# Kernel optimization log

Measured on AMD Instinct MI355X. Metric: run time of the kernel, lower is better.

The kernel has to match this reference:

```python
import jax, jax.numpy as jnp
import numpy as np

H = 512
S = 65  # 64 board cells + appended constant 1


def _heads(y, wk, wq, wv):
    # y: [H, S]; wk/wq/wv: [3, H, H] -> atts: [3, S, H]
    def one(wk_i, wq_i, wv_i):
        k = wk_i @ y            # [H, S]
        q = wq_i @ y            # [H, S]
        v = wv_i @ y            # [H, S]
        sm = jax.nn.softmax(k.T @ q, axis=1)  # [S, S], softmax over dim=1
        return sm @ v.T         # [S, H]
    return jax.vmap(one)(wk, wq, wv)


def setup_inputs() -> dict:
    key = jax.random.key(0)
    ks = jax.random.split(key, 10)
    r = lambda k, s: jax.random.normal(k, s, dtype=jnp.float32)
    return {
        "inputs": r(ks[0], (1, 64)),
        "embedding": r(ks[1], (H, S)),
        "wq": r(ks[2], (3, 3, H, H)),
        "wk": r(ks[3], (3, 3, H, H)),
        "wv": r(ks[4], (3, 3, H, H)),
        "linear1": r(ks[5], (3 * H, H)),
        "linear2": r(ks[6], (3 * H, H)),
        "linear3": r(ks[7], (3 * H, 2 * H)),
        "linear4": r(ks[8], (2 * H, H)),
        "linear5": r(ks[9], (H, 64)),
    }


def reference(inputs, embedding, wq, wk, wv, linear1, linear2, linear3, linear4, linear5):
    x = jnp.concatenate([inputs[0], jnp.ones((1,), inputs.dtype)])  # [S]
    y = embedding * x  # [H, S] (broadcast over rows)

    # Layer 1 (3 heads)
    a1 = _heads(y, wk[0], wq[0], wv[0])  # [3, S, H]
    y = jax.nn.relu(jnp.concatenate([a1[0], a1[1], a1[2]], axis=1) @ linear1).T  # [H, S]

    # Layer 2 -- NOTE: original code cats att11, att12, att23 (a bug we preserve)
    a2 = _heads(y, wk[1], wq[1], wv[1])
    y = jax.nn.relu(jnp.concatenate([a1[0], a1[1], a2[2]], axis=1) @ linear2).T  # [H, S]

    # Layer 3 -- NOTE: original code cats att11, att12, att33 (preserved)
    a3 = _heads(y, wk[2], wq[2], wv[2])
    y = jax.nn.relu(jnp.concatenate([a1[0], a1[1], a3[2]], axis=1) @ linear3)[64]  # [2H]

    # dropout p=0.1 -> identity in eval mode
    y = jnp.tanh(y @ linear4)  # [H]
    score = y @ linear5        # [64]
    return score[None, :]      # [1, 64]
```

## Files before the change

kernel.cpp:

```cpp
#include <hip/hip_runtime.h>
#include <hip/hip_bf16.h>
#include <math.h>

#define H 512
#define S 65
#define SP 80
#define HS (H * S)
#define PHS (H * SP)
#define KS3 24
#define KS4 16


__global__ void scale_embed_kernel(const float* __restrict__ inp,
                                   const float* __restrict__ emb,
                                   float* __restrict__ yT) {
    int i = blockIdx.x * blockDim.x + threadIdx.x;
    if (i < PHS) {
        int s = i / H;
        int h = i % H;
        float v = 0.f;
        if (s < S) {
            float x = (s == 64) ? 1.0f : inp[s];
            v = emb[h * S + s] * x;
        }
        yT[i] = v;
    }
}

__device__ __forceinline__ void mac4(float4& c, float ax, float ay, float az,
                                     float aw, const float4& w0, const float4& w1,
                                     const float4& w2, const float4& w3) {
    c.x = fmaf(ax, w0.x, c.x); c.y = fmaf(ax, w0.y, c.y);
    c.z = fmaf(ax, w0.z, c.z); c.w = fmaf(ax, w0.w, c.w);
    c.x = fmaf(ay, w1.x, c.x); c.y = fmaf(ay, w1.y, c.y);
    c.z = fmaf(ay, w1.z, c.z); c.w = fmaf(ay, w1.w, c.w);
    c.x = fmaf(az, w2.x, c.x); c.y = fmaf(az, w2.y, c.y);
    c.z = fmaf(az, w2.z, c.z); c.w = fmaf(az, w2.w, c.w);
    c.x = fmaf(aw, w3.x, c.x); c.y = fmaf(aw, w3.y, c.y);
    c.z = fmaf(aw, w3.z, c.z); c.w = fmaf(aw, w3.w, c.w);
}

__global__ void __launch_bounds__(256, 1)
kqv_gemm_tiled(const float* __restrict__ wq,
               const float* __restrict__ wk,
               const float* __restrict__ wv,
               int mat0,
               const float* __restrict__ yT,
               float* __restrict__ part) {
    int slot  = blockIdx.z;
    int which = blockIdx.y;
    int mat = mat0 + slot;
    const float* W = (which == 0 ? wk : (which == 1 ? wq : wv)) + (size_t)mat * H * H;

    int n0   = (blockIdx.x & 15) * 32;
    int kidx = blockIdx.x >> 4;

    __shared__ float Wt[64 * 32];
    __shared__ float As[SP * 68];

    int t  = threadIdx.x;
    int nq = t & 7;
    int g  = t >> 3;
    bool r2 = (g < 16);

    float4 acc0 = {0,0,0,0}, acc1 = {0,0,0,0}, acc2 = {0,0,0,0};

    for (int ch = 0; ch < 4; ++ch) {
        int kc0 = kidx * 256 + ch * 64;
#pragma unroll
        for (int c = 0; c < 2; ++c) {
            int f = c * 256 + t;
            int wn  = f >> 4;
            int kf4 = f & 15;
            float4 w4 = *(const float4*)(W + (size_t)(n0 + wn) * H + kc0 + 4 * kf4);
            int sw = ((wn >> 2) ^ (kf4 & 7));
            int base = (4 * kf4) * 32 + 4 * sw + (wn & 3);
            Wt[base     ] = w4.x;
            Wt[base + 32] = w4.y;
            Wt[base + 64] = w4.z;
            Wt[base + 96] = w4.w;
        }
#pragma unroll
        for (int c = 0; c < 5; ++c) {
            int f = c * 256 + t;
            int as  = f >> 4;
            int kf4 = f & 15;
            *(float4*)(&As[as * 68 + 4 * kf4]) =
                *(const float4*)(yT + (size_t)as * H + kc0 + 4 * kf4);
        }
        __syncthreads();

#pragma unroll
        for (int k4 = 0; k4 < 16; ++k4) {
            int swc = 4 * (nq ^ (k4 & 7));
            float4 w0 = *(const float4*)(&Wt[(4 * k4 + 0) * 32 + swc]);
            float4 w1 = *(const float4*)(&Wt[(4 * k4 + 1) * 32 + swc]);
            float4 w2 = *(const float4*)(&Wt[(4 * k4 + 2) * 32 + swc]);
            float4 w3 = *(const float4*)(&Wt[(4 * k4 + 3) * 32 + swc]);
            {
                float4 a = *(const float4*)(&As[g * 68 + 4 * k4]);
                mac4(acc0, a.x, a.y, a.z, a.w, w0, w1, w2, w3);
            }
            {
                float4 a = *(const float4*)(&As[(g + 32) * 68 + 4 * k4]);
                mac4(acc1, a.x, a.y, a.z, a.w, w0, w1, w2, w3);
            }
            if (r2) {
                float4 a = *(const float4*)(&As[(g + 64) * 68 + 4 * k4]);
                mac4(acc2, a.x, a.y, a.z, a.w, w0, w1, w2, w3);
            }
        }
        __syncthreads();
    }

    float* P = part + (size_t)((slot * 3 + which) * 2 + kidx) * PHS;
    *(float4*)(P + (size_t)g * H + n0 + 4 * nq) = acc0;
    *(float4*)(P + (size_t)(g + 32) * H + n0 + 4 * nq) = acc1;
    if (r2) *(float4*)(P + (size_t)(g + 64) * H + n0 + 4 * nq) = acc2;
}

__device__ __forceinline__ float score_part(const float* __restrict__ Q0,
                                            const float* __restrict__ Q1,
                                            const float* __restrict__ ka,
                                            int b, int t) {
    const float4* q0 = (const float4*)(Q0 + (size_t)b * H) + t * 32;
    const float4* q1 = (const float4*)(Q1 + (size_t)b * H) + t * 32;
    const float4* kl = (const float4*)ka + t * 32;
    float4 c0 = {0,0,0,0}, c1 = {0,0,0,0};
#pragma unroll
    for (int u = 0; u < 32; u += 2) {
        float4 qa = q0[u], qb = q1[u], k0 = kl[u];
        float4 qc = q0[u+1], qd = q1[u+1], k1 = kl[u+1];
        c0.x = fmaf(k0.x, qa.x + qb.x, c0.x);
        c0.y = fmaf(k0.y, qa.y + qb.y, c0.y);
        c0.z = fmaf(k0.z, qa.z + qb.z, c0.z);
        c0.w = fmaf(k0.w, qa.w + qb.w, c0.w);
        c1.x = fmaf(k1.x, qc.x + qd.x, c1.x);
        c1.y = fmaf(k1.y, qc.y + qd.y, c1.y);
        c1.z = fmaf(k1.z, qc.z + qd.z, c1.z);
        c1.w = fmaf(k1.w, qc.w + qd.w, c1.w);
    }
    return ((c0.x + c0.y) + (c0.z + c0.w)) + ((c1.x + c1.y) + (c1.z + c1.w));
}

__global__ void attn_kernel(const float* __restrict__ kqvp,
                            float* __restrict__ att) {
    int a = blockIdx.x;
    int slot = blockIdx.y;
    int tid = threadIdx.x;

    const float* base = kqvp + (size_t)slot * 6 * PHS;
    const float* K0 = base;
    const float* K1 = base + PHS;
    const float* Q0 = base + 2 * (size_t)PHS;
    const float* Q1 = base + 3 * (size_t)PHS;
    const float* V0 = base + 4 * (size_t)PHS;
    const float* V1 = base + 5 * (size_t)PHS;
    float* ao = att + (size_t)slot * PHS + (size_t)a * H;

    __shared__ float ka[H];
    __shared__ float sp[4 * 65];
    __shared__ float smv[S];
    __shared__ float p[S];

    ka[tid]       = K0[(size_t)a * H + tid]       + K1[(size_t)a * H + tid];
    ka[tid + 256] = K0[(size_t)a * H + tid + 256] + K1[(size_t)a * H + tid + 256];
    __syncthreads();

    {
        int b = tid & 63;
        int t = tid >> 6;
        sp[t * 65 + b] = score_part(Q0, Q1, ka, b, t);
        if (tid < 4) sp[tid * 65 + 64] = score_part(Q0, Q1, ka, 64, tid);
    }
    __syncthreads();

    if (tid < S) {
        smv[tid] = (sp[tid] + sp[65 + tid]) + (sp[130 + tid] + sp[195 + tid]);
    }
    __syncthreads();

    float maxv = -INFINITY;
    for (int i = 0; i < S; ++i) maxv = fmaxf(maxv, smv[i]);
    float sum = 0.0f;
    for (int i = 0; i < S; ++i) sum += expf(smv[i] - maxv);
    float inv = 1.0f / sum;
    if (tid < S) p[tid] = expf(smv[tid] - maxv) * inv;
    __syncthreads();

#pragma unroll
    for (int rep = 0; rep < 2; ++rep) {
        int hh = tid + rep * 256;
        float a0 = 0.f, a1 = 0.f;
#pragma unroll 4
        for (int b = 0; b < 64; b += 2) {
            a0 = fmaf(p[b    ], V0[(size_t)(b    ) * H + hh] + V1[(size_t)(b    ) * H + hh], a0);
            a1 = fmaf(p[b + 1], V0[(size_t)(b + 1) * H + hh] + V1[(size_t)(b + 1) * H + hh], a1);
        }
        a0 = fmaf(p[64], V0[(size_t)64 * H + hh] + V1[(size_t)64 * H + hh], a0);
        ao[hh] = a0 + a1;
    }
}

__device__ __forceinline__ void lin4row_dev(const float* __restrict__ att,
                                            int col0,
                                            const float* __restrict__ L,
                                            float* __restrict__ dst,
                                            int s0, int tid) {
    __shared__ float Ar[4 * 256];
    __shared__ float4 red[4 * 128];

    {
        int rr = tid >> 6;
        int cc = tid & 63;
        *(float4*)(&Ar[rr * 256 + cc * 4]) =
            *(const float4*)(att + (size_t)(s0 + rr) * H + col0 + cc * 4);
    }
    __syncthreads();

    int h4 = (tid & 127) * 4;
    int jh = tid >> 7;
    const float* Lj = L + (size_t)(jh * 128) * H + h4;
    const float* A0 = Ar + jh * 128;

    float4 c0 = {0,0,0,0}, c1 = {0,0,0,0}, c2 = {0,0,0,0}, c3 = {0,0,0,0};
#pragma unroll 8
    for (int j = 0; j < 128; ++j) {
        float4 L4 = *(const float4*)(Lj + (size_t)j * H);
        float a0 = A0[j], a1 = A0[256 + j], a2 = A0[512 + j], a3 = A0[768 + j];
        c0.x = fmaf(a0, L4.x, c0.x); c0.y = fmaf(a0, L4.y, c0.y);
        c0.z = fmaf(a0, L4.z, c0.z); c0.w = fmaf(a0, L4.w, c0.w);
        c1.x = fmaf(a1, L4.x, c1.x); c1.y = fmaf(a1, L4.y, c1.y);
        c1.z = fmaf(a1, L4.z, c1.z); c1.w = fmaf(a1, L4.w, c1.w);
        c2.x = fmaf(a2, L4.x, c2.x); c2.y = fmaf(a2, L4.y, c2.y);
        c2.z = fmaf(a2, L4.z, c2.z); c2.w = fmaf(a2, L4.w, c2.w);
        c3.x = fmaf(a3, L4.x, c3.x); c3.y = fmaf(a3, L4.y, c3.y);
        c3.z = fmaf(a3, L4.z, c3.z); c3.w = fmaf(a3, L4.w, c3.w);
    }

    if (jh == 1) {
        int x = tid & 127;
        red[x] = c0; red[128 + x] = c1; red[256 + x] = c2; red[384 + x] = c3;
    }
    __syncthreads();
    if (jh == 0) {
        float4 r0 = red[tid], r1 = red[128 + tid], r2 = red[256 + tid], r3 = red[384 + tid];
        c0.x += r0.x; c0.y += r0.y; c0.z += r0.z; c0.w += r0.w;
        c1.x += r1.x; c1.y += r1.y; c1.z += r1.z; c1.w += r1.w;
        c2.x += r2.x; c2.y += r2.y; c2.z += r2.z; c2.w += r2.w;
        c3.x += r3.x; c3.y += r3.y; c3.z += r3.z; c3.w += r3.w;
        *(float4*)(dst + (size_t)(s0 + 0) * H + h4) = c0;
        *(float4*)(dst + (size_t)(s0 + 1) * H + h4) = c1;
        *(float4*)(dst + (size_t)(s0 + 2) * H + h4) = c2;
        *(float4*)(dst + (size_t)(s0 + 3) * H + h4) = c3;
    }
}

__global__ void mega_lin_kernel(const float* __restrict__ att1,
                                const float* __restrict__ lin1,
                                const float* __restrict__ lin2,
                                const float* __restrict__ lin3,
                                float* __restrict__ plin1,
                                float* __restrict__ plin2,
                                float* __restrict__ tpart) {
    int bx = blockIdx.x;
    int tid = threadIdx.x;

    if (bx < 170) {
        int seg = bx / 17;
        int p   = bx % 17;
        const float* att;
        const float* L;
        float* dst;
        if (seg < 6) {
            att = att1 + (size_t)(seg >> 1) * PHS;
            L   = lin1 + (size_t)(seg * 256) * H;
            dst = plin1 + (size_t)seg * PHS;
        } else {
            int s2 = seg - 6;
            att = att1 + (size_t)(s2 >> 1) * PHS;
            L   = lin2 + (size_t)(s2 * 256) * H;
            dst = plin2 + (size_t)s2 * PHS;
        }
        lin4row_dev(att, (seg & 1) * 256, L, dst, p * 4, tid);
    } else {
        int idx = bx - 170;
        int j2 = (idx & 3) * 256 + tid;
        int ks = idx >> 2;
        const float* row = att1 + (size_t)(ks >> 3) * PHS + (size_t)64 * H;
        int j0 = (ks & 7) * 64;
        int jbase = ks * 64;
        float a0 = 0.f, a1 = 0.f, a2 = 0.f, a3 = 0.f;
        for (int j = 0; j < 64; j += 4) {
            a0 = fmaf(row[j0 + j + 0], lin3[(size_t)(jbase + j + 0) * 1024 + j2], a0);
            a1 = fmaf(row[j0 + j + 1], lin3[(size_t)(jbase + j + 1) * 1024 + j2], a1);
            a2 = fmaf(row[j0 + j + 2], lin3[(size_t)(jbase + j + 2) * 1024 + j2], a2);
            a3 = fmaf(row[j0 + j + 3], lin3[(size_t)(jbase + j + 3) * 1024 + j2], a3);
        }
        tpart[ks * 1024 + j2] = (a0 + a1) + (a2 + a3);
    }
}

__global__ void lin2c_kernel(const float* __restrict__ att2,
                             const float* __restrict__ lin2,
                             float* __restrict__ plin2) {
    int seg = 4 + blockIdx.x / 17;
    int p   = blockIdx.x % 17;
    lin4row_dev(att2, (seg & 1) * 256, lin2 + (size_t)(seg * 256) * H,
                plin2 + (size_t)seg * PHS, p * 4, threadIdx.x);
}

__global__ void combine6_relu_kernel(const float* __restrict__ part,
                                     float* __restrict__ yT) {
    int i = blockIdx.x * 256 + threadIdx.x;
    float s = 0.f;
#pragma unroll
    for (int p = 0; p < 6; ++p) s += part[(size_t)p * PHS + i];
    yT[i] = fmaxf(s, 0.0f);
}

__global__ void attn3_lin3c_kernel(const float* __restrict__ kqvp,
                                   const float* __restrict__ lin3,
                                   float* __restrict__ tpart) {
    int tid = threadIdx.x;
    int ks  = 16 + blockIdx.y;
    int j2  = blockIdx.x * 256 + tid;
    int j0  = (ks & 7) * 64;

    const float* K0 = kqvp;
    const float* K1 = kqvp + PHS;
    const float* Q0 = kqvp + 2 * (size_t)PHS;
    const float* Q1 = kqvp + 3 * (size_t)PHS;
    const float* V0 = kqvp + 4 * (size_t)PHS;
    const float* V1 = kqvp + 5 * (size_t)PHS;

    __shared__ float ka[H];
    __shared__ float sp[4 * 65];
    __shared__ float smv[S];
    __shared__ float p[S];
    __shared__ float att_s[64];

    ka[tid]       = K0[(size_t)64 * H + tid]       + K1[(size_t)64 * H + tid];
    ka[tid + 256] = K0[(size_t)64 * H + tid + 256] + K1[(size_t)64 * H + tid + 256];
    __syncthreads();

    {
        int b = tid & 63;
        int t = tid >> 6;
        sp[t * 65 + b] = score_part(Q0, Q1, ka, b, t);
        if (tid < 4) sp[tid * 65 + 64] = score_part(Q0, Q1, ka, 64, tid);
    }
    __syncthreads();

    if (tid < S) {
        smv[tid] = (sp[tid] + sp[65 + tid]) + (sp[130 + tid] + sp[195 + tid]);
    }
    __syncthreads();

    float maxv = -INFINITY;
    for (int i = 0; i < S; ++i) maxv = fmaxf(maxv, smv[i]);
    float sum = 0.0f;
    for (int i = 0; i < S; ++i) sum += expf(smv[i] - maxv);
    float inv = 1.0f / sum;
    if (tid < S) p[tid] = expf(smv[tid] - maxv) * inv;
    __syncthreads();

    if (tid < 64) {
        int hh = j0 + tid;
        float a0 = 0.f, a1 = 0.f;
#pragma unroll 4
        for (int b = 0; b < 64; b += 2) {
            a0 = fmaf(p[b    ], V0[(size_t)(b    ) * H + hh] + V1[(size_t)(b    ) * H + hh], a0);
            a1 = fmaf(p[b + 1], V0[(size_t)(b + 1) * H + hh] + V1[(size_t)(b + 1) * H + hh], a1);
        }
        a0 = fmaf(p[64], V0[(size_t)64 * H + hh] + V1[(size_t)64 * H + hh], a0);
        att_s[tid] = a0 + a1;
    }
    __syncthreads();

    int jbase = ks * 64;
    float a0 = 0.f, a1 = 0.f, a2 = 0.f, a3 = 0.f;
    for (int j = 0; j < 64; j += 4) {
        a0 = fmaf(att_s[j + 0], lin3[(size_t)(jbase + j + 0) * 1024 + j2], a0);
        a1 = fmaf(att_s[j + 1], lin3[(size_t)(jbase + j + 1) * 1024 + j2], a1);
        a2 = fmaf(att_s[j + 2], lin3[(size_t)(jbase + j + 2) * 1024 + j2], a2);
        a3 = fmaf(att_s[j + 3], lin3[(size_t)(jbase + j + 3) * 1024 + j2], a3);
    }
    tpart[ks * 1024 + j2] = (a0 + a1) + (a2 + a3);
}

__global__ void lin4_partial_kernel(const float* __restrict__ tpart,
                                    const float* __restrict__ lin4,
                                    float* __restrict__ upart) {
    __shared__ float tl[64];
    int hh = blockIdx.x * 256 + threadIdx.x;
    int ks = blockIdx.y;
    int j2base = ks * 64;

    if (threadIdx.x < 64) {
        int j2 = j2base + threadIdx.x;
        float s = 0.f;
#pragma unroll
        for (int p = 0; p < KS3; ++p) s += tpart[p * 1024 + j2];
        tl[threadIdx.x] = fmaxf(s, 0.f);
    }
    __syncthreads();

    float a0 = 0.f, a1 = 0.f, a2 = 0.f, a3 = 0.f;
    for (int j = 0; j < 64; j += 4) {
        a0 = fmaf(tl[j + 0], lin4[(size_t)(j2base + j + 0) * H + hh], a0);
        a1 = fmaf(tl[j + 1], lin4[(size_t)(j2base + j + 1) * H + hh], a1);
        a2 = fmaf(tl[j + 2], lin4[(size_t)(j2base + j + 2) * H + hh], a2);
        a3 = fmaf(tl[j + 3], lin4[(size_t)(j2base + j + 3) * H + hh], a3);
    }
    upart[ks * H + hh] = (a0 + a1) + (a2 + a3);
}

__global__ void final_out_kernel(const float* __restrict__ upart,
                                 const float* __restrict__ lin5,
                                 float* __restrict__ out) {
    __shared__ float u[H];
    __shared__ float pr[8][64];
    int tid = threadIdx.x;

    {
        float s = 0.f;
#pragma unroll
        for (int p = 0; p < KS4; ++p) s += upart[p * H + tid];
        u[tid] = tanhf(s);
    }
    __syncthreads();

    int o  = tid & 63;
    int sl = tid >> 6;
    float acc = 0.f;
    int h0 = sl * 64;
#pragma unroll 8
    for (int j = 0; j < 64; ++j) {
        acc = fmaf(u[h0 + j], lin5[(h0 + j) * 64 + o], acc);
    }
    pr[sl][o] = acc;
    __syncthreads();

    if (tid < 64) {
        float s = 0.f;
#pragma unroll
        for (int p = 0; p < 8; ++p) s += pr[p][tid];
        out[tid] = s;
    }
}

extern "C" void kernel_launch(void* const* d_in, const int* in_sizes, int n_in,
                              void* d_out, int out_size, void* d_ws, size_t ws_size,
                              hipStream_t stream) {
    const float* inputs  = (const float*)d_in[0];
    const float* emb     = (const float*)d_in[1];
    const float* wq      = (const float*)d_in[2];
    const float* wk      = (const float*)d_in[3];
    const float* wv      = (const float*)d_in[4];
    const float* linear1 = (const float*)d_in[5];
    const float* linear2 = (const float*)d_in[6];
    const float* linear3 = (const float*)d_in[7];
    const float* linear4 = (const float*)d_in[8];
    const float* linear5 = (const float*)d_in[9];
    float* out = (float*)d_out;

    float* ws    = (float*)d_ws;
    float* y     = ws;
    float* kqvp  = y     + PHS;
    float* att1  = kqvp  + 18 * PHS;
    float* att2  = att1  + 3 * PHS;
    float* plin1 = att2  + PHS;
    float* plin2 = plin1 + 6 * PHS;
    float* tpart = plin2 + 6 * PHS;
    float* upart = tpart + KS3 * 1024;

    const int nb  = HS / 256;
    const int nbp = PHS / 256;

    scale_embed_kernel<<<nbp, 256, 0, stream>>>(inputs, emb, y);

    kqv_gemm_tiled<<<dim3(32, 3, 3), 256, 0, stream>>>(wq, wk, wv, 0, y, kqvp);
    attn_kernel<<<dim3(S, 3), 256, 0, stream>>>(kqvp, att1);
    mega_lin_kernel<<<234, 256, 0, stream>>>(att1, linear1, linear2, linear3,
                                             plin1, plin2, tpart);
    combine6_relu_kernel<<<nb, 256, 0, stream>>>(plin1, y);

    kqv_gemm_tiled<<<dim3(32, 3, 1), 256, 0, stream>>>(wq, wk, wv, 5, y, kqvp);
    attn_kernel<<<dim3(S, 1), 256, 0, stream>>>(kqvp, att2);
    lin2c_kernel<<<34, 256, 0, stream>>>(att2, linear2, plin2);
    combine6_relu_kernel<<<nb, 256, 0, stream>>>(plin2, y);

    kqv_gemm_tiled<<<dim3(32, 3, 1), 256, 0, stream>>>(wq, wk, wv, 8, y, kqvp);
    attn3_lin3c_kernel<<<dim3(4, 8), 256, 0, stream>>>(kqvp, linear3, tpart);

    lin4_partial_kernel<<<dim3(2, KS4), 256, 0, stream>>>(tpart, linear4, upart);
    final_out_kernel<<<1, 512, 0, stream>>>(upart, linear5, out);
}
```

Measured before the change: 254.8 us.

## Drop K-split for layer-1 KQV GEMM and fuse lin2 tail with combine

```diff
diff --git a/kernel.cpp b/kernel.cpp
--- a/kernel.cpp
+++ b/kernel.cpp
@@ -40,6 +40,7 @@
     c.z = fmaf(aw, w3.z, c.z); c.w = fmaf(aw, w3.w, c.w);
 }
 
+template <int KSPLIT>
 __global__ void __launch_bounds__(256, 1)
 kqv_gemm_tiled(const float* __restrict__ wq,
                const float* __restrict__ wk,
@@ -54,6 +55,7 @@
 
     int n0   = (blockIdx.x & 15) * 32;
     int kidx = blockIdx.x >> 4;
+    const int NCH = 8 / KSPLIT;
 
     __shared__ float Wt[64 * 32];
     __shared__ float As[SP * 68];
@@ -65,8 +67,8 @@
 
     float4 acc0 = {0,0,0,0}, acc1 = {0,0,0,0}, acc2 = {0,0,0,0};
 
-    for (int ch = 0; ch < 4; ++ch) {
-        int kc0 = kidx * 256 + ch * 64;
+    for (int ch = 0; ch < NCH; ++ch) {
+        int kc0 = (kidx * NCH + ch) * 64;
 #pragma unroll
         for (int c = 0; c < 2; ++c) {
             int f = c * 256 + t;
@@ -113,49 +115,54 @@
         __syncthreads();
     }
 
-    float* P = part + (size_t)((slot * 3 + which) * 2 + kidx) * PHS;
+    float* P = part + (size_t)((slot * 3 + which) * KSPLIT + kidx) * PHS;
     *(float4*)(P + (size_t)g * H + n0 + 4 * nq) = acc0;
     *(float4*)(P + (size_t)(g + 32) * H + n0 + 4 * nq) = acc1;
     if (r2) *(float4*)(P + (size_t)(g + 64) * H + n0 + 4 * nq) = acc2;
 }
 
-__device__ __forceinline__ float score_part(const float* __restrict__ Q0,
-                                            const float* __restrict__ Q1,
+template <int NS>
+__device__ __forceinline__ float score_part(const float* __restrict__ Q,
                                             const float* __restrict__ ka,
                                             int b, int t) {
-    const float4* q0 = (const float4*)(Q0 + (size_t)b * H) + t * 32;
-    const float4* q1 = (const float4*)(Q1 + (size_t)b * H) + t * 32;
+    const float4* q0 = (const float4*)(Q + (size_t)b * H) + t * 32;
+    const float4* q1 = (const float4*)(Q + PHS + (size_t)b * H) + t * 32;
     const float4* kl = (const float4*)ka + t * 32;
     float4 c0 = {0,0,0,0}, c1 = {0,0,0,0};
 #pragma unroll
     for (int u = 0; u < 32; u += 2) {
-        float4 qa = q0[u], qb = q1[u], k0 = kl[u];
-        float4 qc = q0[u+1], qd = q1[u+1], k1 = kl[u+1];
-        c0.x = fmaf(k0.x, qa.x + qb.x, c0.x);
-        c0.y = fmaf(k0.y, qa.y + qb.y, c0.y);
-        c0.z = fmaf(k0.z, qa.z + qb.z, c0.z);
-        c0.w = fmaf(k0.w, qa.w + qb.w, c0.w);
-        c1.x = fmaf(k1.x, qc.x + qd.x, c1.x);
-        c1.y = fmaf(k1.y, qc.y + qd.y, c1.y);
-        c1.z = fmaf(k1.z, qc.z + qd.z, c1.z);
-        c1.w = fmaf(k1.w, qc.w + qd.w, c1.w);
+        float4 qa = q0[u], qc = q0[u + 1];
+        float4 k0 = kl[u], k1 = kl[u + 1];
+        if (NS == 2) {
+            float4 qb = q1[u], qd = q1[u + 1];
+            qa.x += qb.x; qa.y += qb.y; qa.z += qb.z; qa.w += qb.w;
+            qc.x += qd.x; qc.y += qd.y; qc.z += qd.z; qc.w += qd.w;
+        }
+        c0.x = fmaf(k0.x, qa.x, c0.x);
+        c0.y = fmaf(k0.y, qa.y, c0.y);
+        c0.z = fmaf(k0.z, qa.z, c0.z);
+        c0.w = fmaf(k0.w, qa.w, c0.w);
+        c1.x = fmaf(k1.x, qc.x, c1.x);
+        c1.y = fmaf(k1.y, qc.y, c1.y);
+        c1.z = fmaf(k1.z, qc.z, c1.z);
+        c1.w = fmaf(k1.w, qc.w, c1.w);
     }
     return ((c0.x + c0.y) + (c0.z + c0.w)) + ((c1.x + c1.y) + (c1.z + c1.w));
 }
 
+template <int NS>
 __global__ void attn_kernel(const float* __restrict__ kqvp,
                             float* __restrict__ att) {
     int a = blockIdx.x;
     int slot = blockIdx.y;
     int tid = threadIdx.x;
 
-    const float* base = kqvp + (size_t)slot * 6 * PHS;
+    const float* base = kqvp + (size_t)slot * 3 * NS * PHS;
     const float* K0 = base;
-    const float* K1 = base + PHS;
-    const float* Q0 = base + 2 * (size_t)PHS;
-    const float* Q1 = base + 3 * (size_t)PHS;
-    const float* V0 = base + 4 * (size_t)PHS;
-    const float* V1 = base + 5 * (size_t)PHS;
+    const float* Q0 = base + (size_t)NS * PHS;
+    const float* V0 = base + (size_t)2 * NS * PHS;
+    const float* K1 = K0 + PHS;
+    const float* V1 = V0 + PHS;
     float* ao = att + (size_t)slot * PHS + (size_t)a * H;
 
     __shared__ float ka[H];
@@ -163,15 +170,20 @@
     __shared__ float smv[S];
     __shared__ float p[S];
 
-    ka[tid]       = K0[(size_t)a * H + tid]       + K1[(size_t)a * H + tid];
-    ka[tid + 256] = K0[(size_t)a * H + tid + 256] + K1[(size_t)a * H + tid + 256];
+    if (NS == 2) {
+        ka[tid]       = K0[(size_t)a * H + tid]       + K1[(size_t)a * H + tid];
+        ka[tid + 256] = K0[(size_t)a * H + tid + 256] + K1[(size_t)a * H + tid + 256];
+    } else {
+        ka[tid]       = K0[(size_t)a * H + tid];
+        ka[tid + 256] = K0[(size_t)a * H + tid + 256];
+    }
     __syncthreads();
 
     {
         int b = tid & 63;
         int t = tid >> 6;
-        sp[t * 65 + b] = score_part(Q0, Q1, ka, b, t);
-        if (tid < 4) sp[tid * 65 + 64] = score_part(Q0, Q1, ka, 64, tid);
+        sp[t * 65 + b] = score_part<NS>(Q0, ka, b, t);
+        if (tid < 4) sp[tid * 65 + 64] = score_part<NS>(Q0, ka, 64, tid);
     }
     __syncthreads();
 
@@ -194,10 +206,20 @@
         float a0 = 0.f, a1 = 0.f;
 #pragma unroll 4
         for (int b = 0; b < 64; b += 2) {
-            a0 = fmaf(p[b    ], V0[(size_t)(b    ) * H + hh] + V1[(size_t)(b    ) * H + hh], a0);
-            a1 = fmaf(p[b + 1], V0[(size_t)(b + 1) * H + hh] + V1[(size_t)(b + 1) * H + hh], a1);
-        }
-        a0 = fmaf(p[64], V0[(size_t)64 * H + hh] + V1[(size_t)64 * H + hh], a0);
+            float v0 = V0[(size_t)(b    ) * H + hh];
+            float v1 = V0[(size_t)(b + 1) * H + hh];
+            if (NS == 2) {
+                v0 += V1[(size_t)(b    ) * H + hh];
+                v1 += V1[(size_t)(b + 1) * H + hh];
+            }
+            a0 = fmaf(p[b    ], v0, a0);
+            a1 = fmaf(p[b + 1], v1, a1);
+        }
+        {
+            float v0 = V0[(size_t)64 * H + hh];
+            if (NS == 2) v0 += V1[(size_t)64 * H + hh];
+            a0 = fmaf(p[64], v0, a0);
+        }
         ao[hh] = a0 + a1;
     }
 }
@@ -301,15 +323,6 @@
     }
 }
 
-__global__ void lin2c_kernel(const float* __restrict__ att2,
-                             const float* __restrict__ lin2,
-                             float* __restrict__ plin2) {
-    int seg = 4 + blockIdx.x / 17;
-    int p   = blockIdx.x % 17;
-    lin4row_dev(att2, (seg & 1) * 256, lin2 + (size_t)(seg * 256) * H,
-                plin2 + (size_t)seg * PHS, p * 4, threadIdx.x);
-}
-
 __global__ void combine6_relu_kernel(const float* __restrict__ part,
                                      float* __restrict__ yT) {
     int i = blockIdx.x * 256 + threadIdx.x;
@@ -317,6 +330,35 @@
 #pragma unroll
     for (int p = 0; p < 6; ++p) s += part[(size_t)p * PHS + i];
     yT[i] = fmaxf(s, 0.0f);
+}
+
+__global__ void lin2c_combine_kernel(const float* __restrict__ att2,
+                                     const float* __restrict__ lin2,
+                                     const float* __restrict__ plin2,
+                                     float* __restrict__ yT) {
+    int i = blockIdx.x * 256 + threadIdx.x;
+    int s = i / H;
+    int h = i % H;
+    const float* row = att2 + (size_t)s * H;
+    const float* L4 = lin2 + (size_t)1024 * H + h;
+    const float* L5 = lin2 + (size_t)1280 * H + h;
+
+    float a0 = 0.f, a1 = 0.f, a2 = 0.f, a3 = 0.f;
+    for (int j = 0; j < 256; j += 4) {
+        a0 = fmaf(row[j + 0], L4[(size_t)(j + 0) * H], a0);
+        a1 = fmaf(row[j + 1], L4[(size_t)(j + 1) * H], a1);
+        a2 = fmaf(row[j + 2], L4[(size_t)(j + 2) * H], a2);
+        a3 = fmaf(row[j + 3], L4[(size_t)(j + 3) * H], a3);
+    }
+    for (int j = 0; j < 256; j += 4) {
+        a0 = fmaf(row[256 + j + 0], L5[(size_t)(j + 0) * H], a0);
+        a1 = fmaf(row[256 + j + 1], L5[(size_t)(j + 1) * H], a1);
+        a2 = fmaf(row[256 + j + 2], L5[(size_t)(j + 2) * H], a2);
+        a3 = fmaf(row[256 + j + 3], L5[(size_t)(j + 3) * H], a3);
+    }
+    float tot = (a0 + a1) + (a2 + a3)
+              + plin2[i] + plin2[PHS + i] + plin2[2 * PHS + i] + plin2[3 * PHS + i];
+    yT[i] = fmaxf(tot, 0.0f);
 }
 
 __global__ void attn3_lin3c_kernel(const float* __restrict__ kqvp,
@@ -330,7 +372,6 @@
     const float* K0 = kqvp;
     const float* K1 = kqvp + PHS;
     const float* Q0 = kqvp + 2 * (size_t)PHS;
-    const float* Q1 = kqvp + 3 * (size_t)PHS;
     const float* V0 = kqvp + 4 * (size_t)PHS;
     const float* V1 = kqvp + 5 * (size_t)PHS;
 
@@ -347,8 +388,8 @@
     {
         int b = tid & 63;
         int t = tid >> 6;
-        sp[t * 65 + b] = score_part(Q0, Q1, ka, b, t);
-        if (tid < 4) sp[tid * 65 + 64] = score_part(Q0, Q1, ka, 64, tid);
+        sp[t * 65 + b] = score_part<2>(Q0, ka, b, t);
+        if (tid < 4) sp[tid * 65 + 64] = score_part<2>(Q0, ka, 64, tid);
     }
     __syncthreads();
 
@@ -468,11 +509,11 @@
     float* ws    = (float*)d_ws;
     float* y     = ws;
     float* kqvp  = y     + PHS;
-    float* att1  = kqvp  + 18 * PHS;
+    float* att1  = kqvp  + 9 * PHS;
     float* att2  = att1  + 3 * PHS;
     float* plin1 = att2  + PHS;
     float* plin2 = plin1 + 6 * PHS;
-    float* tpart = plin2 + 6 * PHS;
+    float* tpart = plin2 + 4 * PHS;
     float* upart = tpart + KS3 * 1024;
 
     const int nb  = HS / 256;
@@ -480,18 +521,17 @@
 
     scale_embed_kernel<<<nbp, 256, 0, stream>>>(inputs, emb, y);
 
-    kqv_gemm_tiled<<<dim3(32, 3, 3), 256, 0, stream>>>(wq, wk, wv, 0, y, kqvp);
-    attn_kernel<<<dim3(S, 3), 256, 0, stream>>>(kqvp, att1);
+    kqv_gemm_tiled<1><<<dim3(16, 3, 3), 256, 0, stream>>>(wq, wk, wv, 0, y, kqvp);
+    attn_kernel<1><<<dim3(S, 3), 256, 0, stream>>>(kqvp, att1);
     mega_lin_kernel<<<234, 256, 0, stream>>>(att1, linear1, linear2, linear3,
                                              plin1, plin2, tpart);
     combine6_relu_kernel<<<nb, 256, 0, stream>>>(plin1, y);
 
-    kqv_gemm_tiled<<<dim3(32, 3, 1), 256, 0, stream>>>(wq, wk, wv, 5, y, kqvp);
-    attn_kernel<<<dim3(S, 1), 256, 0, stream>>>(kqvp, att2);
-    lin2c_kernel<<<34, 256, 0, stream>>>(att2, linear2, plin2);
-    combine6_relu_kernel<<<nb, 256, 0, stream>>>(plin2, y);
-
-    kqv_gemm_tiled<<<dim3(32, 3, 1), 256, 0, stream>>>(wq, wk, wv, 8, y, kqvp);
+    kqv_gemm_tiled<2><<<dim3(32, 3, 1), 256, 0, stream>>>(wq, wk, wv, 5, y, kqvp);
+    attn_kernel<2><<<dim3(S, 1), 256, 0, stream>>>(kqvp, att2);
+    lin2c_combine_kernel<<<nb, 256, 0, stream>>>(att2, linear2, plin2, y);
+
+    kqv_gemm_tiled<2><<<dim3(32, 3, 1), 256, 0, stream>>>(wq, wk, wv, 8, y, kqvp);
     attn3_lin3c_kernel<<<dim3(4, 8), 256, 0, stream>>>(kqvp, linear3, tpart);
 
     lin4_partial_kernel<<<dim3(2, KS4), 256, 0, stream>>>(tpart, linear4, upart);
```

New measurement: 259.4 us. Within noise of the previous version (+1.8%).
